# Performance work log

Hardware: AMD Instinct MI355X
Metric: run time of the kernel (lower is better)

The kernel has to match this reference:

```python
import jax, jax.numpy as jnp
import numpy as np
from jax import lax

B, A, T, D, V, K = 16, 1024, 512, 256, 50000, 3
EXP_DILS = [1, 2, 4, 8, 16, 32, 32]  # conv_num=7, exp_num=5
REF_DILS = [1, 1, 1]                 # refine_num=3


def setup_inputs() -> dict:
    key = jax.random.key(0)
    ks = jax.random.split(key, 14)
    inp = {
        'article_word': jax.random.randint(ks[0], (B, A), 0, V),
        'article_char': jax.random.randint(ks[1], (B, A, 16), 0, 100),
        'template_word': jax.random.randint(ks[2], (B, T), 0, V),
        'template_char': jax.random.randint(ks[3], (B, T, 16), 0, 100),
        'article_mask': jnp.ones((B, A), jnp.float32),
        'template_mask': jnp.ones((B, T), jnp.float32),
        'emb': jax.random.normal(ks[4], (V, D), jnp.float32) * 0.02,
        'exp_w': jax.random.normal(ks[5], (7, K, D, 2 * D), jnp.float32) * 0.03,
        'exp_b': jnp.zeros((7, 2 * D), jnp.float32),
        'ref_w': jax.random.normal(ks[6], (3, K, D, 2 * D), jnp.float32) * 0.03,
        'ref_b': jnp.zeros((3, 2 * D), jnp.float32),
        'ff1_w': jax.random.normal(ks[7], (10, 10), jnp.float32) * 0.3,
        'ff1_b': jnp.zeros((10,), jnp.float32),
        'ff2_w': jax.random.normal(ks[8], (10, 1), jnp.float32) * 0.3,
        'ff2_b': jnp.zeros((1,), jnp.float32),
    }
    return inp


def _res_block(x, w, b, dilation):
    # x: [B, L, D]; w: [K, D, 2D]  (Conv1d, padding='same' given k//2*dilation)
    pad = (K // 2) * dilation
    y = lax.conv_general_dilated(x, w, window_strides=(1,), padding=[(pad, pad)],
                                 rhs_dilation=(dilation,),
                                 dimension_numbers=('NWC', 'WIO', 'NWC')) + b
    a, g = jnp.split(y, 2, axis=2)  # GLU on channel dim
    return x + a * jax.nn.sigmoid(g)


def _encode(x, exp_w, exp_b, ref_w, ref_b):
    for i, d in enumerate(EXP_DILS):
        x = _res_block(x, exp_w[i], exp_b[i], d)
    for i, d in enumerate(REF_DILS):
        x = _res_block(x, ref_w[i], ref_b[i], d)
    return x  # dropout is identity in eval mode


def reference(article_word, article_char, template_word, template_char,
              article_mask, template_mask, emb, exp_w, exp_b, ref_w, ref_b,
              ff1_w, ff1_b, ff2_w, ff2_b):
    art = _encode(emb[article_word], exp_w, exp_b, ref_w, ref_b)    # [B,A,D]
    tpl = _encode(emb[template_word], exp_w, exp_b, ref_w, ref_b)   # [B,T,D]
    # pairwise squared distance without materializing [B,A,T,D]
    a2 = jnp.sum(art * art, axis=-1)                 # [B,A]
    t2 = jnp.sum(tpl * tpl, axis=-1)                 # [B,T]
    dot = jnp.einsum('bad,btd->bat', art, tpl)       # [B,A,T]
    dist = jnp.maximum(a2[:, :, None] + t2[:, None, :] - 2.0 * dot, 0.0)
    S = jnp.exp(-dist) * article_mask[:, :, None] * template_mask[:, None, :]
    row_max = jnp.max(S, axis=2)                     # [B,A]
    top, _ = lax.top_k(row_max, 10)                  # sorted descending, [B,10]
    h = jax.nn.relu(top @ ff1_w + ff1_b)             # [B,10]
    out = (h @ ff2_w + ff2_b).squeeze()              # [B]
    return out
```

## Files before the change

kernel.cpp:

```cpp
#include <hip/hip_runtime.h>
#include <math.h>

#define NB 16
#define NA 1024
#define NT 512
#define ND 256
#define PAD 32

typedef short bf8_t __attribute__((ext_vector_type(8)));
typedef float f4_t __attribute__((ext_vector_type(4)));

__device__ __forceinline__ float bf2f(ushort u) {
    union { unsigned int i; float f; } v; v.i = ((unsigned int)u) << 16; return v.f;
}
__device__ __forceinline__ ushort f2bf(float f) {
    union { float f; unsigned int i; } v; v.f = f;
    unsigned int x = v.i;
    unsigned int r = (x + 0x7fffu + ((x >> 16) & 1u)) >> 16;
    return (ushort)r;
}
__device__ __forceinline__ void gl_lds16(const void* g, void* l) {
    __builtin_amdgcn_global_load_lds(
        (const __attribute__((address_space(1))) unsigned int*)g,
        (__attribute__((address_space(3))) unsigned int*)l, 16, 0, 0);
}


__global__ void prep_kernel(const int* __restrict__ art_w, const int* __restrict__ tpl_w,
                            const float* __restrict__ emb,
                            ushort* __restrict__ art_a, ushort* __restrict__ art_b,
                            ushort* __restrict__ tpl_a, ushort* __restrict__ tpl_b) {
    int idx = blockIdx.x * 256 + threadIdx.x;
    if (idx < NB * 32 * NA) {
        int l = idx & (NA - 1);
        int bq = idx >> 10;
        int qq = bq & 31, b = bq >> 5;
        int wd = art_w[b * NA + l];
        const float4* src = (const float4*)(emb + (size_t)wd * ND + qq * 8);
        float4 v0 = src[0], v1 = src[1];
        ushort o[8];
        o[0]=f2bf(v0.x); o[1]=f2bf(v0.y); o[2]=f2bf(v0.z); o[3]=f2bf(v0.w);
        o[4]=f2bf(v1.x); o[5]=f2bf(v1.y); o[6]=f2bf(v1.z); o[7]=f2bf(v1.w);
        *(uint4*)(art_a + ((size_t)bq * (NA + 64) + PAD + l) * 8) = *(uint4*)o;
    } else if (idx < NB * 32 * NA + NB * 32 * NT) {
        int j = idx - NB * 32 * NA;
        int l = j & (NT - 1);
        int bq = j >> 9;
        int qq = bq & 31, b = bq >> 5;
        int wd = tpl_w[b * NT + l];
        const float4* src = (const float4*)(emb + (size_t)wd * ND + qq * 8);
        float4 v0 = src[0], v1 = src[1];
        ushort o[8];
        o[0]=f2bf(v0.x); o[1]=f2bf(v0.y); o[2]=f2bf(v0.z); o[3]=f2bf(v0.w);
        o[4]=f2bf(v1.x); o[5]=f2bf(v1.y); o[6]=f2bf(v1.z); o[7]=f2bf(v1.w);
        *(uint4*)(tpl_a + ((size_t)bq * (NT + 64) + PAD + l) * 8) = *(uint4*)o;
    } else {
        int j = idx - (NB * 32 * NA + NB * 32 * NT);
        int y = j >> 15;
        int rem = j & 32767;
        ushort* p = (y == 0) ? art_a : (y == 1) ? art_b : (y == 2) ? tpl_a : tpl_b;
        int L = (y < 2) ? NA : NT;
        int Lp = L + 2 * PAD;
        int plane = rem >> 6;
        int row_in = rem & 63;
        int slab = (row_in < PAD) ? row_in : L + row_in;
        uint4 z = make_uint4(0, 0, 0, 0);
        *(uint4*)(p + ((size_t)plane * Lp + slab) * 8) = z;
    }
}

__global__ void __launch_bounds__(256)
repack_w(const float* __restrict__ exp_w, const float* __restrict__ ref_w,
         ushort* __restrict__ wpack) {
    __shared__ float tile[64][65];
    int li = blockIdx.z;
    int gk = blockIdx.x;
    int gc = blockIdx.y;
    const float* src = (li < 7) ? exp_w + (size_t)li * 3 * ND * 512
                                : ref_w + (size_t)(li - 7) * 3 * ND * 512;
    int k0g = gk * 64, c0 = gc * 64;
    int tid = threadIdx.x;
    #pragma unroll
    for (int p = 0; p < 4; ++p) {
        int kr = p * 16 + (tid >> 4);
        int cc = (tid & 15) * 4;
        *(float4*)&tile[kr][cc] =
            *(const float4*)(src + (size_t)(k0g + kr) * 512 + c0 + cc);
    }
    __syncthreads();
    int tap = k0g >> 8, kl0 = k0g & 255, kc0 = kl0 >> 5;
    int ag = c0 >> 8, cb = (c0 & 255) >> 6;
    int kg = tid >> 5, idx = tid & 31;
    int kc = kc0 + (kg >> 2), qq = kg & 3;
    #pragma unroll
    for (int h = 0; h < 2; ++h) {
        int w64 = idx + h * 32;
        int cprime = h * 64 + ag * 32 + idx;
        ushort o[8];
        #pragma unroll
        for (int j = 0; j < 8; ++j) o[j] = f2bf(tile[kg * 8 + j][w64]);
        ushort* d = wpack +
            (((((size_t)(li * 4 + cb) * 3 + tap) * 8 + kc) * 4 + qq) * 128 + cprime) * 8;
        *(uint4*)d = *(uint4*)o;
    }
}

__global__ void __launch_bounds__(256, 4)
conv_glu_mfma(const ushort* __restrict__ art_x, ushort* __restrict__ art_y,
              const ushort* __restrict__ tpl_x, ushort* __restrict__ tpl_y,
              const ushort* __restrict__ wp, const float* __restrict__ bias,
              int dil) {
    __shared__ char smem[34816];
    ushort* Als = (ushort*)smem;
    float* ylds = (float*)smem;

    const int tid = threadIdx.x;
    const int w = tid >> 6, lane = tid & 63;
    const int wm = w >> 1, wn = w & 1;
    const int q = lane >> 4, l15 = lane & 15;

    const int id = blockIdx.x;
    const int cb = (id >> 3) & 3;
    const int pb = ((id >> 5) << 3) | (id & 7);
    const int plane = pb % 12;
    const int b = pb / 12;
    const int b32 = b * 32;

    int Lp, l0;
    const ushort* xb;
    ushort* yb;
    if (plane < 8) {
        Lp = NA + 2 * PAD; l0 = plane * 128;
        xb = art_x; yb = art_y;
    } else {
        Lp = NT + 2 * PAD; l0 = (plane - 8) * 128;
        xb = tpl_x; yb = tpl_y;
    }
    const ushort* wl = wp + (size_t)cb * 98304;
    const int boff = (q * 128 + wn * 64 + l15) * 8;

    f4_t acc[4][4];
    #pragma unroll
    for (int i = 0; i < 4; ++i)
        #pragma unroll
        for (int j = 0; j < 4; ++j)
            acc[i][j] = (f4_t){0.f, 0.f, 0.f, 0.f};

    for (int kc2 = 0; kc2 < 4; ++kc2) {
        #pragma unroll
        for (int s3 = 0; s3 < 6; ++s3) {
            int s = w + s3 * 4;
            int h = s / 12, within = s % 12;
            int qq = kc2 * 8 + h * 4 + within / 3;
            int rphys = l0 + (within % 3) * 64 + lane;
            gl_lds16(xb + ((size_t)(b32 + qq) * Lp + rphys) * 8, Als + s * 512);
        }
        __syncthreads();

        #pragma unroll
        for (int h = 0; h < 2; ++h) {
            const int kc = kc2 * 2 + h;
            const ushort* wkc = wl + kc * 4096 + boff;
            const ushort* Ah = Als + h * 6144;
            #pragma unroll
            for (int t = 0; t < 3; ++t) {
                bf8_t bfr[4];
                #pragma unroll
                for (int nt = 0; nt < 4; ++nt)
                    bfr[nt] = *(const bf8_t*)(wkc + t * 32768 + nt * 128);
                const int sh = (t - 1) * dil;
                bf8_t af[4];
                #pragma unroll
                for (int mt = 0; mt < 4; ++mt)
                    af[mt] = *(const bf8_t*)(Ah + (q * 192 + 32 + sh + wm * 64 + mt * 16 + l15) * 8);
                #pragma unroll
                for (int mt = 0; mt < 4; ++mt)
                    #pragma unroll
                    for (int nt = 0; nt < 4; ++nt)
                        acc[mt][nt] = __builtin_amdgcn_mfma_f32_16x16x32_bf16(
                            af[mt], bfr[nt], acc[mt][nt], 0, 0, 0);
            }
        }
        __syncthreads();
    }

    #pragma unroll
    for (int nt = 0; nt < 2; ++nt) {
        const int cl = wn * 32 + nt * 16 + l15;
        const int chan = cb * 64 + cl;
        const float ba = bias[chan];
        const float bg2 = bias[chan + 256];
        #pragma unroll
        for (int mt = 0; mt < 4; ++mt) {
            #pragma unroll
            for (int r = 0; r < 4; ++r) {
                const int row = wm * 64 + mt * 16 + q * 4 + r;
                float av = acc[mt][nt][r] + ba;
                float gv = acc[mt][nt + 2][r] + bg2;
                ylds[row * 68 + cl] = av / (1.f + __expf(-gv));
            }
        }
    }
    __syncthreads();

    #pragma unroll
    for (int p = 0; p < 4; ++p) {
        int u = p * 256 + tid;
        int cl8 = u >> 7;
        int row = u & 127;
        size_t go = ((size_t)(b32 + cb * 8 + cl8) * Lp + l0 + PAD + row) * 8;
        ushort xv[8]; *(uint4*)xv = *(const uint4*)(xb + go);
        float4 y0 = *(float4*)&ylds[row * 68 + cl8 * 8];
        float4 y1 = *(float4*)&ylds[row * 68 + cl8 * 8 + 4];
        ushort ov[8];
        ov[0]=f2bf(bf2f(xv[0])+y0.x); ov[1]=f2bf(bf2f(xv[1])+y0.y);
        ov[2]=f2bf(bf2f(xv[2])+y0.z); ov[3]=f2bf(bf2f(xv[3])+y0.w);
        ov[4]=f2bf(bf2f(xv[4])+y1.x); ov[5]=f2bf(bf2f(xv[5])+y1.y);
        ov[6]=f2bf(bf2f(xv[6])+y1.z); ov[7]=f2bf(bf2f(xv[7])+y1.w);
        *(uint4*)(yb + go) = *(uint4*)ov;
    }
}

__global__ void sumsq_bf16(const ushort* __restrict__ art, const ushort* __restrict__ tpl,
                           float* __restrict__ a2, float* __restrict__ t2) {
    __shared__ float red[4][64];
    int which = blockIdx.y;
    if (which == 1 && blockIdx.x >= 128) return;
    const ushort* x = which ? tpl : art;
    float* out = which ? t2 : a2;
    int L = which ? NT : NA;
    int Lp = L + 2 * PAD;
    int tid = threadIdx.x;
    int r = tid & 63, pg = tid >> 6;
    int row_g = blockIdx.x * 64 + r;
    int b = row_g / L, l = row_g - b * L;
    float s = 0.f;
    #pragma unroll
    for (int j = 0; j < 8; ++j) {
        int qq = pg * 8 + j;
        const ushort* p = x + ((size_t)(b * 32 + qq) * Lp + PAD + l) * 8;
        ushort v[8]; *(uint4*)v = *(const uint4*)p;
        #pragma unroll
        for (int e = 0; e < 8; ++e) { float f = bf2f(v[e]); s += f * f; }
    }
    red[pg][r] = s;
    __syncthreads();
    if (tid < 64)
        out[blockIdx.x * 64 + tid] =
            red[0][tid] + red[1][tid] + red[2][tid] + red[3][tid];
}

__global__ void __launch_bounds__(256, 4)
dist_rowmax_mfma(const ushort* __restrict__ art, const ushort* __restrict__ tpl,
                 const float* __restrict__ a2, const float* __restrict__ t2,
                 const float* __restrict__ amask, const float* __restrict__ tmask,
                 float* __restrict__ rmaxp) {
    __shared__ ushort Als[64 * 32];
    __shared__ ushort Bls[128 * 32];
    __shared__ float red[2][64];

    const int tid = threadIdx.x;
    const int w = tid >> 6, lane = tid & 63;
    const int wm = w >> 1, wn = w & 1;
    const int q = lane >> 4, l15 = lane & 15;

    const int id = blockIdx.x;
    const int b = (id & 7) | (((id >> 3) & 1) << 3);
    const int rest = id >> 4;
    const int a0 = (rest & 15) * 64;
    const int tplane = rest >> 4;
    const int t0 = tplane * 128;
    const int b32 = b * 32;
    const int LpA = NA + 2 * PAD, LpT = NT + 2 * PAD;

    float a2v[2][4], amv[2][4];
    #pragma unroll
    for (int mt = 0; mt < 2; ++mt)
        #pragma unroll
        for (int r = 0; r < 4; ++r) {
            int row = a0 + wm * 32 + mt * 16 + q * 4 + r;
            a2v[mt][r] = a2[b * NA + row];
            amv[mt][r] = amask[b * NA + row];
        }

    f4_t acc[2][4];
    #pragma unroll
    for (int i = 0; i < 2; ++i)
        #pragma unroll
        for (int j = 0; j < 4; ++j)
            acc[i][j] = (f4_t){0.f, 0.f, 0.f, 0.f};

    for (int kb = 0; kb < 8; ++kb) {
        #pragma unroll
        for (int s3 = 0; s3 < 3; ++s3) {
            int s = w + s3 * 4;
            if (s < 4) {
                int qq = kb * 4 + s;
                gl_lds16(art + ((size_t)(b32 + qq) * LpA + PAD + a0 + lane) * 8,
                         Als + s * 512);
            } else {
                int s2 = s - 4;
                int qq = kb * 4 + (s2 >> 1);
                int r0 = (s2 & 1) * 64;
                gl_lds16(tpl + ((size_t)(b32 + qq) * LpT + PAD + t0 + r0 + lane) * 8,
                         Bls + s2 * 512);
            }
        }
        __syncthreads();

        bf8_t af[2], bfr[4];
        #pragma unroll
        for (int mt = 0; mt < 2; ++mt)
            af[mt] = *(const bf8_t*)(Als + (q * 64 + wm * 32 + mt * 16 + l15) * 8);
        #pragma unroll
        for (int nt = 0; nt < 4; ++nt)
            bfr[nt] = *(const bf8_t*)(Bls + (q * 128 + wn * 64 + nt * 16 + l15) * 8);
        #pragma unroll
        for (int mt = 0; mt < 2; ++mt)
            #pragma unroll
            for (int nt = 0; nt < 4; ++nt)
                acc[mt][nt] = __builtin_amdgcn_mfma_f32_16x16x32_bf16(
                    af[mt], bfr[nt], acc[mt][nt], 0, 0, 0);
        __syncthreads();
    }

    float rm[2][4];
    #pragma unroll
    for (int mt = 0; mt < 2; ++mt)
        #pragma unroll
        for (int r = 0; r < 4; ++r) rm[mt][r] = 0.f;

    #pragma unroll
    for (int nt = 0; nt < 4; ++nt) {
        int t = t0 + wn * 64 + nt * 16 + l15;
        float t2v = t2[b * NT + t];
        float tmv = tmask[b * NT + t];
        #pragma unroll
        for (int mt = 0; mt < 2; ++mt)
            #pragma unroll
            for (int r = 0; r < 4; ++r) {
                float d = a2v[mt][r] + t2v - 2.f * acc[mt][nt][r];
                d = fmaxf(d, 0.f);
                float s = __expf(-d) * amv[mt][r] * tmv;
                rm[mt][r] = fmaxf(rm[mt][r], s);
            }
    }
    #pragma unroll
    for (int mt = 0; mt < 2; ++mt)
        #pragma unroll
        for (int r = 0; r < 4; ++r) {
            float v = rm[mt][r];
            #pragma unroll
            for (int off = 1; off < 16; off <<= 1)
                v = fmaxf(v, __shfl_xor(v, off));
            rm[mt][r] = v;
        }
    if (l15 == 0) {
        #pragma unroll
        for (int mt = 0; mt < 2; ++mt)
            #pragma unroll
            for (int r = 0; r < 4; ++r)
                red[wn][wm * 32 + mt * 16 + q * 4 + r] = rm[mt][r];
    }
    __syncthreads();
    if (tid < 64)
        rmaxp[((size_t)tplane * NB + b) * NA + a0 + tid] =
            fmaxf(red[0][tid], red[1][tid]);
}

__global__ void __launch_bounds__(256)
topk_mlp_kernel(const float* __restrict__ rmaxp,
                const float* __restrict__ ff1_w, const float* __restrict__ ff1_b,
                const float* __restrict__ ff2_w, const float* __restrict__ ff2_b,
                float* __restrict__ out) {
    __shared__ float vals[NA];
    __shared__ float top[10];
    __shared__ float h[10];
    __shared__ float rv[4];
    __shared__ int ri[4];

    int b = blockIdx.x;
    int tid = threadIdx.x;
    int lane = tid & 63, wv = tid >> 6;
    for (int i = tid; i < NA; i += 256) {
        float m = rmaxp[(size_t)b * NA + i];
        m = fmaxf(m, rmaxp[((size_t)NB + b) * NA + i]);
        m = fmaxf(m, rmaxp[((size_t)2 * NB + b) * NA + i]);
        m = fmaxf(m, rmaxp[((size_t)3 * NB + b) * NA + i]);
        vals[i] = m;
    }
    __syncthreads();

    for (int it = 0; it < 10; ++it) {
        float best = -1e30f;
        int bi = 0;
        #pragma unroll
        for (int u = 0; u < 4; ++u) {
            int i = u * 256 + tid;
            if (vals[i] > best) { best = vals[i]; bi = i; }
        }
        #pragma unroll
        for (int off = 32; off; off >>= 1) {
            float ob = __shfl_down(best, off);
            int oi = __shfl_down(bi, off);
            if (ob > best) { best = ob; bi = oi; }
        }
        if (lane == 0) { rv[wv] = best; ri[wv] = bi; }
        __syncthreads();
        if (tid == 0) {
            float bb = rv[0]; int bbi = ri[0];
            #pragma unroll
            for (int k = 1; k < 4; ++k)
                if (rv[k] > bb) { bb = rv[k]; bbi = ri[k]; }
            top[it] = bb; vals[bbi] = -1e30f;
        }
        __syncthreads();
    }

    if (tid < 10) {
        float s = ff1_b[tid];
        #pragma unroll
        for (int i = 0; i < 10; ++i) s += top[i] * ff1_w[i * 10 + tid];
        h[tid] = fmaxf(s, 0.f);
    }
    __syncthreads();
    if (tid == 0) {
        float s = ff2_b[0];
        #pragma unroll
        for (int j = 0; j < 10; ++j) s += h[j] * ff2_w[j];
        out[b] = s;
    }
}

extern "C" void kernel_launch(void* const* d_in, const int* in_sizes, int n_in,
                              void* d_out, int out_size, void* d_ws, size_t ws_size,
                              hipStream_t stream) {
    const int*   art_w = (const int*)d_in[0];
    const int*   tpl_w = (const int*)d_in[2];
    const float* amask = (const float*)d_in[4];
    const float* tmask = (const float*)d_in[5];
    const float* emb   = (const float*)d_in[6];
    const float* exp_w = (const float*)d_in[7];
    const float* exp_b = (const float*)d_in[8];
    const float* ref_w = (const float*)d_in[9];
    const float* ref_b = (const float*)d_in[10];
    const float* ff1_w = (const float*)d_in[11];
    const float* ff1_b = (const float*)d_in[12];
    const float* ff2_w = (const float*)d_in[13];
    const float* ff2_b = (const float*)d_in[14];
    float* out = (float*)d_out;

    const size_t art_bytes = (size_t)NB * 32 * (NA + 2 * PAD) * 8 * 2;
    const size_t tpl_bytes = (size_t)NB * 32 * (NT + 2 * PAD) * 8 * 2;
    const size_t wpk_bytes = (size_t)10 * 4 * 3 * 8 * 4 * 128 * 8 * 2;

    char* p = (char*)d_ws;
    ushort* art_a = (ushort*)p; p += art_bytes;
    ushort* art_b = (ushort*)p; p += art_bytes;
    ushort* tpl_a = (ushort*)p; p += tpl_bytes;
    ushort* tpl_b = (ushort*)p; p += tpl_bytes;
    ushort* wpack = (ushort*)p; p += wpk_bytes;
    float* a2    = (float*)p; p += (size_t)NB * NA * 4;
    float* t2    = (float*)p; p += (size_t)NB * NT * 4;
    float* rmaxp = (float*)p; p += (size_t)4 * NB * NA * 4;

    repack_w<<<dim3(12, 8, 10), 256, 0, stream>>>(exp_w, ref_w, wpack);
    {
        int n = NB * 32 * NA + NB * 32 * NT + 4 * NB * 32 * 64;
        prep_kernel<<<(n + 255) / 256, 256, 0, stream>>>(
            art_w, tpl_w, emb, art_a, art_b, tpl_a, tpl_b);
    }

    const int dils[10] = {1, 2, 4, 8, 16, 32, 32, 1, 1, 1};

    ushort* a_cur = art_a; ushort* a_nxt = art_b;
    ushort* t_cur = tpl_a; ushort* t_nxt = tpl_b;
    for (int i = 0; i < 10; ++i) {
        const ushort* wl = wpack + (size_t)i * 4 * 98304;
        const float* bb = (i < 7) ? exp_b + (size_t)i * 512
                                  : ref_b + (size_t)(i - 7) * 512;
        conv_glu_mfma<<<768, 256, 0, stream>>>(
            a_cur, a_nxt, t_cur, t_nxt, wl, bb, dils[i]);
        ushort* t1 = a_cur; a_cur = a_nxt; a_nxt = t1;
        ushort* t2p = t_cur; t_cur = t_nxt; t_nxt = t2p;
    }
    ushort* art_fin = a_cur;
    ushort* tpl_fin = t_cur;

    sumsq_bf16<<<dim3(256, 2), 256, 0, stream>>>(art_fin, tpl_fin, a2, t2);

    dist_rowmax_mfma<<<1024, 256, 0, stream>>>(
        art_fin, tpl_fin, a2, t2, amask, tmask, rmaxp);

    topk_mlp_kernel<<<NB, 256, 0, stream>>>(rmaxp, ff1_w, ff1_b, ff2_w, ff2_b, out);
}
```

Baseline: 382.5 us.

## Double-buffer LDS loads in conv and distance kernels; fuse setup and sumsq

Result: slower. 404.1 us (+5.7%).

```diff
diff --git a/kernel.cpp b/kernel.cpp
--- a/kernel.cpp
+++ b/kernel.cpp
@@ -26,12 +26,20 @@
 }
 
 
-__global__ void prep_kernel(const int* __restrict__ art_w, const int* __restrict__ tpl_w,
-                            const float* __restrict__ emb,
-                            ushort* __restrict__ art_a, ushort* __restrict__ art_b,
-                            ushort* __restrict__ tpl_a, ushort* __restrict__ tpl_b) {
-    int idx = blockIdx.x * 256 + threadIdx.x;
-    if (idx < NB * 32 * NA) {
+__global__ void __launch_bounds__(256)
+setup_kernel(const int* __restrict__ art_w, const int* __restrict__ tpl_w,
+             const float* __restrict__ emb,
+             ushort* __restrict__ art_a, ushort* __restrict__ art_b,
+             ushort* __restrict__ tpl_a, ushort* __restrict__ tpl_b,
+             const float* __restrict__ exp_w, const float* __restrict__ ref_w,
+             ushort* __restrict__ wpack,
+             float* __restrict__ a2, float* __restrict__ t2) {
+    __shared__ float tile[64][65];
+    int bid = blockIdx.x;
+    int tid = threadIdx.x;
+
+    if (bid < 2048) {
+        int idx = bid * 256 + tid;
         int l = idx & (NA - 1);
         int bq = idx >> 10;
         int qq = bq & 31, b = bq >> 5;
@@ -42,8 +50,11 @@
         o[0]=f2bf(v0.x); o[1]=f2bf(v0.y); o[2]=f2bf(v0.z); o[3]=f2bf(v0.w);
         o[4]=f2bf(v1.x); o[5]=f2bf(v1.y); o[6]=f2bf(v1.z); o[7]=f2bf(v1.w);
         *(uint4*)(art_a + ((size_t)bq * (NA + 64) + PAD + l) * 8) = *(uint4*)o;
-    } else if (idx < NB * 32 * NA + NB * 32 * NT) {
-        int j = idx - NB * 32 * NA;
+        return;
+    }
+    bid -= 2048;
+    if (bid < 1024) {
+        int j = bid * 256 + tid;
         int l = j & (NT - 1);
         int bq = j >> 9;
         int qq = bq & 31, b = bq >> 5;
@@ -54,8 +65,11 @@
         o[0]=f2bf(v0.x); o[1]=f2bf(v0.y); o[2]=f2bf(v0.z); o[3]=f2bf(v0.w);
         o[4]=f2bf(v1.x); o[5]=f2bf(v1.y); o[6]=f2bf(v1.z); o[7]=f2bf(v1.w);
         *(uint4*)(tpl_a + ((size_t)bq * (NT + 64) + PAD + l) * 8) = *(uint4*)o;
-    } else {
-        int j = idx - (NB * 32 * NA + NB * 32 * NT);
+        return;
+    }
+    bid -= 1024;
+    if (bid < 512) {
+        int j = bid * 256 + tid;
         int y = j >> 15;
         int rem = j & 32767;
         ushort* p = (y == 0) ? art_a : (y == 1) ? art_b : (y == 2) ? tpl_a : tpl_b;
@@ -66,42 +80,48 @@
         int slab = (row_in < PAD) ? row_in : L + row_in;
         uint4 z = make_uint4(0, 0, 0, 0);
         *(uint4*)(p + ((size_t)plane * Lp + slab) * 8) = z;
-    }
-}
-
-__global__ void __launch_bounds__(256)
-repack_w(const float* __restrict__ exp_w, const float* __restrict__ ref_w,
-         ushort* __restrict__ wpack) {
-    __shared__ float tile[64][65];
-    int li = blockIdx.z;
-    int gk = blockIdx.x;
-    int gc = blockIdx.y;
-    const float* src = (li < 7) ? exp_w + (size_t)li * 3 * ND * 512
-                                : ref_w + (size_t)(li - 7) * 3 * ND * 512;
-    int k0g = gk * 64, c0 = gc * 64;
-    int tid = threadIdx.x;
-    #pragma unroll
-    for (int p = 0; p < 4; ++p) {
-        int kr = p * 16 + (tid >> 4);
-        int cc = (tid & 15) * 4;
-        *(float4*)&tile[kr][cc] =
-            *(const float4*)(src + (size_t)(k0g + kr) * 512 + c0 + cc);
-    }
-    __syncthreads();
-    int tap = k0g >> 8, kl0 = k0g & 255, kc0 = kl0 >> 5;
-    int ag = c0 >> 8, cb = (c0 & 255) >> 6;
-    int kg = tid >> 5, idx = tid & 31;
-    int kc = kc0 + (kg >> 2), qq = kg & 3;
-    #pragma unroll
-    for (int h = 0; h < 2; ++h) {
-        int w64 = idx + h * 32;
-        int cprime = h * 64 + ag * 32 + idx;
-        ushort o[8];
-        #pragma unroll
-        for (int j = 0; j < 8; ++j) o[j] = f2bf(tile[kg * 8 + j][w64]);
-        ushort* d = wpack +
-            (((((size_t)(li * 4 + cb) * 3 + tap) * 8 + kc) * 4 + qq) * 128 + cprime) * 8;
-        *(uint4*)d = *(uint4*)o;
+        return;
+    }
+    bid -= 512;
+    if (bid < 24) {
+        int i = (bid * 256 + tid) * 4;
+        float4 z = make_float4(0.f, 0.f, 0.f, 0.f);
+        if (i < NB * NA) *(float4*)(a2 + i) = z;
+        else             *(float4*)(t2 + i - NB * NA) = z;
+        return;
+    }
+    bid -= 24;
+    {
+        int li = bid / 96;
+        int r = bid % 96;
+        int gk = r >> 3;
+        int gc = r & 7;
+        const float* src = (li < 7) ? exp_w + (size_t)li * 3 * ND * 512
+                                    : ref_w + (size_t)(li - 7) * 3 * ND * 512;
+        int k0g = gk * 64, c0 = gc * 64;
+        #pragma unroll
+        for (int p = 0; p < 4; ++p) {
+            int kr = p * 16 + (tid >> 4);
+            int cc = (tid & 15) * 4;
+            *(float4*)&tile[kr][cc] =
+                *(const float4*)(src + (size_t)(k0g + kr) * 512 + c0 + cc);
+        }
+        __syncthreads();
+        int tap = k0g >> 8, kl0 = k0g & 255, kc0 = kl0 >> 5;
+        int ag = c0 >> 8, cb = (c0 & 255) >> 6;
+        int kg = tid >> 5, idx = tid & 31;
+        int kc = kc0 + (kg >> 2), qq = kg & 3;
+        #pragma unroll
+        for (int h = 0; h < 2; ++h) {
+            int w64 = idx + h * 32;
+            int cprime = h * 64 + ag * 32 + idx;
+            ushort o[8];
+            #pragma unroll
+            for (int j = 0; j < 8; ++j) o[j] = f2bf(tile[kg * 8 + j][w64]);
+            ushort* d = wpack +
+                (((((size_t)(li * 4 + cb) * 3 + tap) * 8 + kc) * 4 + qq) * 128 + cprime) * 8;
+            *(uint4*)d = *(uint4*)o;
+        }
     }
 }
 
@@ -109,9 +129,9 @@
 conv_glu_mfma(const ushort* __restrict__ art_x, ushort* __restrict__ art_y,
               const ushort* __restrict__ tpl_x, ushort* __restrict__ tpl_y,
               const ushort* __restrict__ wp, const float* __restrict__ bias,
-              int dil) {
+              int dil, int last, float* __restrict__ a2, float* __restrict__ t2) {
     __shared__ char smem[34816];
-    ushort* Als = (ushort*)smem;
+    ushort* Abuf = (ushort*)smem;
     float* ylds = (float*)smem;
 
     const int tid = threadIdx.x;
@@ -129,12 +149,14 @@
     int Lp, l0;
     const ushort* xb;
     ushort* yb;
+    float* sq;
+    int sqbase;
     if (plane < 8) {
         Lp = NA + 2 * PAD; l0 = plane * 128;
-        xb = art_x; yb = art_y;
+        xb = art_x; yb = art_y; sq = a2; sqbase = b * NA + l0;
     } else {
         Lp = NT + 2 * PAD; l0 = (plane - 8) * 128;
-        xb = tpl_x; yb = tpl_y;
+        xb = tpl_x; yb = tpl_y; sq = t2; sqbase = b * NT + l0;
     }
     const ushort* wl = wp + (size_t)cb * 98304;
     const int boff = (q * 128 + wn * 64 + l15) * 8;
@@ -146,43 +168,48 @@
         for (int j = 0; j < 4; ++j)
             acc[i][j] = (f4_t){0.f, 0.f, 0.f, 0.f};
 
-    for (int kc2 = 0; kc2 < 4; ++kc2) {
-        #pragma unroll
-        for (int s3 = 0; s3 < 6; ++s3) {
-            int s = w + s3 * 4;
-            int h = s / 12, within = s % 12;
-            int qq = kc2 * 8 + h * 4 + within / 3;
-            int rphys = l0 + (within % 3) * 64 + lane;
-            gl_lds16(xb + ((size_t)(b32 + qq) * Lp + rphys) * 8, Als + s * 512);
-        }
-        __syncthreads();
-
-        #pragma unroll
-        for (int h = 0; h < 2; ++h) {
-            const int kc = kc2 * 2 + h;
-            const ushort* wkc = wl + kc * 4096 + boff;
-            const ushort* Ah = Als + h * 6144;
-            #pragma unroll
-            for (int t = 0; t < 3; ++t) {
-                bf8_t bfr[4];
+    #pragma unroll
+    for (int s3 = 0; s3 < 3; ++s3) {
+        int s = w + s3 * 4;
+        int qq = s / 3;
+        int rphys = l0 + (s % 3) * 64 + lane;
+        gl_lds16(xb + ((size_t)(b32 + qq) * Lp + rphys) * 8, Abuf + s * 512);
+    }
+
+    for (int kc = 0; kc < 8; ++kc) {
+        __syncthreads();
+        if (kc < 7) {
+            ushort* dst = Abuf + ((kc + 1) & 1) * 6144;
+            #pragma unroll
+            for (int s3 = 0; s3 < 3; ++s3) {
+                int s = w + s3 * 4;
+                int qq = (kc + 1) * 4 + s / 3;
+                int rphys = l0 + (s % 3) * 64 + lane;
+                gl_lds16(xb + ((size_t)(b32 + qq) * Lp + rphys) * 8, dst + s * 512);
+            }
+        }
+        const ushort* Ah = Abuf + (kc & 1) * 6144;
+        const ushort* wkc = wl + kc * 4096 + boff;
+        #pragma unroll
+        for (int t = 0; t < 3; ++t) {
+            bf8_t bfr[4];
+            #pragma unroll
+            for (int nt = 0; nt < 4; ++nt)
+                bfr[nt] = *(const bf8_t*)(wkc + t * 32768 + nt * 128);
+            const int sh = (t - 1) * dil;
+            bf8_t af[4];
+            #pragma unroll
+            for (int mt = 0; mt < 4; ++mt)
+                af[mt] = *(const bf8_t*)(Ah + (q * 192 + 32 + sh + wm * 64 + mt * 16 + l15) * 8);
+            #pragma unroll
+            for (int mt = 0; mt < 4; ++mt)
                 #pragma unroll
                 for (int nt = 0; nt < 4; ++nt)
-                    bfr[nt] = *(const bf8_t*)(wkc + t * 32768 + nt * 128);
-                const int sh = (t - 1) * dil;
-                bf8_t af[4];
-                #pragma unroll
-                for (int mt = 0; mt < 4; ++mt)
-                    af[mt] = *(const bf8_t*)(Ah + (q * 192 + 32 + sh + wm * 64 + mt * 16 + l15) * 8);
-                #pragma unroll
-                for (int mt = 0; mt < 4; ++mt)
-                    #pragma unroll
-                    for (int nt = 0; nt < 4; ++nt)
-                        acc[mt][nt] = __builtin_amdgcn_mfma_f32_16x16x32_bf16(
-                            af[mt], bfr[nt], acc[mt][nt], 0, 0, 0);
-            }
-        }
-        __syncthreads();
-    }
+                    acc[mt][nt] = __builtin_amdgcn_mfma_f32_16x16x32_bf16(
+                        af[mt], bfr[nt], acc[mt][nt], 0, 0, 0);
+        }
+    }
+    __syncthreads();
 
     #pragma unroll
     for (int nt = 0; nt < 2; ++nt) {
@@ -203,6 +230,7 @@
     }
     __syncthreads();
 
+    float ss = 0.f;
     #pragma unroll
     for (int p = 0; p < 4; ++p) {
         int u = p * 256 + tid;
@@ -218,36 +246,19 @@
         ov[4]=f2bf(bf2f(xv[4])+y1.x); ov[5]=f2bf(bf2f(xv[5])+y1.y);
         ov[6]=f2bf(bf2f(xv[6])+y1.z); ov[7]=f2bf(bf2f(xv[7])+y1.w);
         *(uint4*)(yb + go) = *(uint4*)ov;
-    }
-}
-
-__global__ void sumsq_bf16(const ushort* __restrict__ art, const ushort* __restrict__ tpl,
-                           float* __restrict__ a2, float* __restrict__ t2) {
-    __shared__ float red[4][64];
-    int which = blockIdx.y;
-    if (which == 1 && blockIdx.x >= 128) return;
-    const ushort* x = which ? tpl : art;
-    float* out = which ? t2 : a2;
-    int L = which ? NT : NA;
-    int Lp = L + 2 * PAD;
-    int tid = threadIdx.x;
-    int r = tid & 63, pg = tid >> 6;
-    int row_g = blockIdx.x * 64 + r;
-    int b = row_g / L, l = row_g - b * L;
-    float s = 0.f;
-    #pragma unroll
-    for (int j = 0; j < 8; ++j) {
-        int qq = pg * 8 + j;
-        const ushort* p = x + ((size_t)(b * 32 + qq) * Lp + PAD + l) * 8;
-        ushort v[8]; *(uint4*)v = *(const uint4*)p;
-        #pragma unroll
-        for (int e = 0; e < 8; ++e) { float f = bf2f(v[e]); s += f * f; }
-    }
-    red[pg][r] = s;
-    __syncthreads();
-    if (tid < 64)
-        out[blockIdx.x * 64 + tid] =
-            red[0][tid] + red[1][tid] + red[2][tid] + red[3][tid];
+        if (last) {
+            #pragma unroll
+            for (int j = 0; j < 8; ++j) { float f = bf2f(ov[j]); ss += f * f; }
+        }
+    }
+    if (last) {
+        float* ssred = (float*)smem;
+        __syncthreads();
+        ssred[tid] = ss;
+        __syncthreads();
+        if (tid < 128)
+            atomicAdd(&sq[sqbase + tid], ssred[tid] + ssred[tid + 128]);
+    }
 }
 
 __global__ void __launch_bounds__(256, 4)
@@ -255,8 +266,8 @@
                  const float* __restrict__ a2, const float* __restrict__ t2,
                  const float* __restrict__ amask, const float* __restrict__ tmask,
                  float* __restrict__ rmaxp) {
-    __shared__ ushort Als[64 * 32];
-    __shared__ ushort Bls[128 * 32];
+    __shared__ ushort Als[2][4 * 512];
+    __shared__ ushort Bls[2][8 * 512];
     __shared__ float red[2][64];
 
     const int tid = threadIdx.x;
@@ -290,38 +301,56 @@
         for (int j = 0; j < 4; ++j)
             acc[i][j] = (f4_t){0.f, 0.f, 0.f, 0.f};
 
+    #pragma unroll
+    for (int s3 = 0; s3 < 3; ++s3) {
+        int s = w + s3 * 4;
+        if (s < 4) {
+            gl_lds16(art + ((size_t)(b32 + s) * LpA + PAD + a0 + lane) * 8,
+                     Als[0] + s * 512);
+        } else {
+            int s2 = s - 4;
+            int qq = s2 >> 1;
+            int r0 = (s2 & 1) * 64;
+            gl_lds16(tpl + ((size_t)(b32 + qq) * LpT + PAD + t0 + r0 + lane) * 8,
+                     Bls[0] + s2 * 512);
+        }
+    }
+
     for (int kb = 0; kb < 8; ++kb) {
-        #pragma unroll
-        for (int s3 = 0; s3 < 3; ++s3) {
-            int s = w + s3 * 4;
-            if (s < 4) {
-                int qq = kb * 4 + s;
-                gl_lds16(art + ((size_t)(b32 + qq) * LpA + PAD + a0 + lane) * 8,
-                         Als + s * 512);
-            } else {
-                int s2 = s - 4;
-                int qq = kb * 4 + (s2 >> 1);
-                int r0 = (s2 & 1) * 64;
-                gl_lds16(tpl + ((size_t)(b32 + qq) * LpT + PAD + t0 + r0 + lane) * 8,
-                         Bls + s2 * 512);
+        __syncthreads();
+        if (kb < 7) {
+            int nb = (kb + 1) & 1;
+            #pragma unroll
+            for (int s3 = 0; s3 < 3; ++s3) {
+                int s = w + s3 * 4;
+                if (s < 4) {
+                    int qq = (kb + 1) * 4 + s;
+                    gl_lds16(art + ((size_t)(b32 + qq) * LpA + PAD + a0 + lane) * 8,
+                             Als[nb] + s * 512);
+                } else {
+                    int s2 = s - 4;
+                    int qq = (kb + 1) * 4 + (s2 >> 1);
+                    int r0 = (s2 & 1) * 64;
+                    gl_lds16(tpl + ((size_t)(b32 + qq) * LpT + PAD + t0 + r0 + lane) * 8,
+                             Bls[nb] + s2 * 512);
+                }
             }
         }
-        __syncthreads();
-
+        const ushort* Ab = Als[kb & 1];
+        const ushort* Bb = Bls[kb & 1];
         bf8_t af[2], bfr[4];
         #pragma unroll
         for (int mt = 0; mt < 2; ++mt)
-            af[mt] = *(const bf8_t*)(Als + (q * 64 + wm * 32 + mt * 16 + l15) * 8);
+            af[mt] = *(const bf8_t*)(Ab + (q * 64 + wm * 32 + mt * 16 + l15) * 8);
         #pragma unroll
         for (int nt = 0; nt < 4; ++nt)
-            bfr[nt] = *(const bf8_t*)(Bls + (q * 128 + wn * 64 + nt * 16 + l15) * 8);
+            bfr[nt] = *(const bf8_t*)(Bb + (q * 128 + wn * 64 + nt * 16 + l15) * 8);
         #pragma unroll
         for (int mt = 0; mt < 2; ++mt)
             #pragma unroll
             for (int nt = 0; nt < 4; ++nt)
                 acc[mt][nt] = __builtin_amdgcn_mfma_f32_16x16x32_bf16(
                     af[mt], bfr[nt], acc[mt][nt], 0, 0, 0);
-        __syncthreads();
     }
 
     float rm[2][4];
@@ -464,12 +493,9 @@
     float* t2    = (float*)p; p += (size_t)NB * NT * 4;
     float* rmaxp = (float*)p; p += (size_t)4 * NB * NA * 4;
 
-    repack_w<<<dim3(12, 8, 10), 256, 0, stream>>>(exp_w, ref_w, wpack);
-    {
-        int n = NB * 32 * NA + NB * 32 * NT + 4 * NB * 32 * 64;
-        prep_kernel<<<(n + 255) / 256, 256, 0, stream>>>(
-            art_w, tpl_w, emb, art_a, art_b, tpl_a, tpl_b);
-    }
+    setup_kernel<<<4568, 256, 0, stream>>>(art_w, tpl_w, emb,
+                                           art_a, art_b, tpl_a, tpl_b,
+                                           exp_w, ref_w, wpack, a2, t2);
 
     const int dils[10] = {1, 2, 4, 8, 16, 32, 32, 1, 1, 1};
 
@@ -480,15 +506,13 @@
         const float* bb = (i < 7) ? exp_b + (size_t)i * 512
                                   : ref_b + (size_t)(i - 7) * 512;
         conv_glu_mfma<<<768, 256, 0, stream>>>(
-            a_cur, a_nxt, t_cur, t_nxt, wl, bb, dils[i]);
+            a_cur, a_nxt, t_cur, t_nxt, wl, bb, dils[i], (i == 9) ? 1 : 0, a2, t2);
         ushort* t1 = a_cur; a_cur = a_nxt; a_nxt = t1;
         ushort* t2p = t_cur; t_cur = t_nxt; t_nxt = t2p;
     }
     ushort* art_fin = a_cur;
     ushort* tpl_fin = t_cur;
 
-    sumsq_bf16<<<dim3(256, 2), 256, 0, stream>>>(art_fin, tpl_fin, a2, t2);
-
     dist_rowmax_mfma<<<1024, 256, 0, stream>>>(
         art_fin, tpl_fin, a2, t2, amask, tmask, rmaxp);
 
```
